# Kernel optimization log

Hardware: AMD Instinct MI355X
Metric: run time of the kernel (lower is better)

Reference implementation:

```python
import jax, jax.numpy as jnp
import numpy as np

V_PATCH_NUMS = (1, 2, 3, 4, 5, 6, 8, 10, 13, 16)


def _pool_matrix(in_size: int, out_size: int) -> jnp.ndarray:
    # Matrix form of torch adaptive_avg_pool1d (== F.interpolate mode='area'):
    # window i averages input bins [floor(i*in/out), ceil((i+1)*in/out)).
    M = np.zeros((out_size, in_size), dtype=np.float32)
    for i in range(out_size):
        s = (i * in_size) // out_size
        e = -((-(i + 1) * in_size) // out_size)  # ceil division
        M[i, s:e] = 1.0 / (e - s)
    return jnp.asarray(M)


def setup_inputs() -> dict:
    key = jax.random.key(0)
    k1, k2 = jax.random.split(key)
    B, C, H, W = 64, 32, 16, 16
    vocab = 4096
    f = jax.random.normal(k1, (B, C, H, W), dtype=jnp.float32)
    # embedding init: uniform(-1/vocab, 1/vocab), as in the torch module
    emb = (jax.random.uniform(k2, (vocab, C), dtype=jnp.float32) * 2.0 - 1.0) / vocab
    return {"f": f, "emb": emb}


def reference(f, emb):
    # Multi-scale residual VQ: per scale -> area-downsample residual,
    # nearest-codebook argmin, embedding gather, bicubic-upsample,
    # accumulate into f_hat and subtract from f_rest.
    B, C, H, W = f.shape
    f = jax.lax.stop_gradient(f)            # f_no_grad in torch
    x = jnp.transpose(f, (0, 2, 3, 1))      # BHWC for resize/gather
    f_rest = x
    f_hat = jnp.zeros_like(x)
    emb_ng = jax.lax.stop_gradient(emb)     # distances use embedding.weight.data
    e_sq = jnp.sum(emb_ng * emb_ng, axis=1)  # [vocab]
    SN = len(V_PATCH_NUMS)
    for si, pn in enumerate(V_PATCH_NUMS):
        last = si == SN - 1
        if last:
            z = f_rest                       # [B,H,W,C]
        else:
            Mh = _pool_matrix(H, pn)
            Mw = _pool_matrix(W, pn)
            z = jnp.einsum('ph,qw,bhwc->bpqc', Mh, Mw, f_rest)  # area interp
        z_NC = z.reshape(-1, C)
        # squared L2 distance to every code: ||z||^2 + ||e||^2 - 2 z e^T
        d = jnp.sum(z_NC * z_NC, axis=1, keepdims=True) + e_sq - 2.0 * (z_NC @ emb_ng.T)
        idx = jnp.argmin(d, axis=1).reshape(B, pn, pn)
        h = emb[idx]                         # [B,pn,pn,C] gather (grad-carrying emb)
        if not last:
            h = jax.image.resize(h, (B, H, W, C), method='cubic')  # bicubic up
        f_hat = f_hat + h
        f_rest = f_rest - h
    return jnp.transpose(f_hat, (0, 3, 1, 2))  # back to BCHW
```

## Files before the change

kernel.cpp:

```cpp
#include <hip/hip_runtime.h>
#include <math.h>

#define WS_ESQ   0
#define WS_STATE 4096
#define WS_FHAT  (4096 + 524288)
#define WS_Z     (4096 + 2*524288)
#define WS_PSC   (4096 + 3*524288)
#define WS_PIX   (4096 + 3*524288 + 131072)

__device__ __forceinline__ float4 v4add(float4 a, float4 b) {
    return make_float4(__fadd_rn(a.x,b.x), __fadd_rn(a.y,b.y),
                       __fadd_rn(a.z,b.z), __fadd_rn(a.w,b.w));
}
__device__ __forceinline__ float4 v4sq(float4 a) {
    return make_float4(__fmul_rn(a.x,a.x), __fmul_rn(a.y,a.y),
                       __fmul_rn(a.z,a.z), __fmul_rn(a.w,a.w));
}
__device__ __forceinline__ float np_pw32(float4 q0, float4 q1, float4 q2, float4 q3,
                                         float4 q4, float4 q5, float4 q6, float4 q7) {
    float4 rA = v4add(v4add(v4add(q0, q2), q4), q6);
    float4 rB = v4add(v4add(v4add(q1, q3), q5), q7);
    float l = __fadd_rn(__fadd_rn(rA.x, rA.y), __fadd_rn(rA.z, rA.w));
    float h = __fadd_rn(__fadd_rn(rB.x, rB.y), __fadd_rn(rB.z, rB.w));
    return __fadd_rn(l, h);
}

__device__ __forceinline__ double keys64(double x) {
    if (x < 1.0)      return ((1.5*x - 2.5)*x)*x + 1.0;
    else if (x < 2.0) return ((-0.5*x + 2.5)*x - 4.0)*x + 2.0;
    return 0.0;
}

__global__ __launch_bounds__(256) void vq_apply(
    const float* __restrict__ f, const float* __restrict__ emb,
    float* __restrict__ esq, float* __restrict__ state, float* __restrict__ fhat,
    float* __restrict__ zws, const float* __restrict__ psc, const int* __restrict__ pix,
    int sIdx, int pn, int pnPrev, int ncbPrev)
{
    __shared__ float fr[1280];
    __shared__ float hs[676];
    __shared__ int   idx_arr[176];
    __shared__ float U[256];
    __shared__ float red_f[1360];
    __shared__ int   red_i[1360];

    const int tid = threadIdx.x;
    const int wg  = blockIdx.x;
    if (wg >= 512) {
        int j = ((wg - 512) << 8) + tid;
        const float4* e4 = (const float4*)(emb + (size_t)j*32);
        esq[j] = np_pw32(v4sq(e4[0]),v4sq(e4[1]),v4sq(e4[2]),v4sq(e4[3]),
                         v4sq(e4[4]),v4sq(e4[5]),v4sq(e4[6]),v4sq(e4[7]));
        return;
    }
    const int b  = wg >> 3;
    const int c0 = (wg & 7) * 4;

    const float* src = (sIdx <= 1) ? f : state;
    for (int o = tid; o < 1024; o += 256) {
        int cc = o >> 8, yx = o & 255;
        fr[yx*5 + cc] = src[b*8192 + (c0 + cc)*256 + yx];
    }
    __syncthreads();

    if (sIdx > 0) {
        const int Vp = pnPrev * pnPrev;
        const int step = ncbPrev >> 3;
        for (int t = tid; t < Vp*8; t += 256) {
            int v = t >> 3, k = t & 7;
            const size_t base = (size_t)((v << 6) + b) * ncbPrev;
            float best = INFINITY; int bi = 0;
            for (int ch = k*step; ch < (k+1)*step; ++ch) {
                float sc = psc[base + ch];
                if (sc < best) { best = sc; bi = pix[base + ch]; }
            }
            red_f[t] = best; red_i[t] = bi;
        }
        __syncthreads();
        if (tid < Vp) {
            float best = INFINITY; int bi = 0;
            for (int k = 0; k < 8; ++k) {
                float sc = red_f[tid*8 + k];
                if (sc < best) { best = sc; bi = red_i[tid*8 + k]; }
            }
            idx_arr[tid] = bi;
        }
        __syncthreads();
        for (int t = tid; t < Vp*4; t += 256)
            hs[t] = emb[(size_t)idx_arr[t >> 2]*32 + c0 + (t & 3)];
        if (tid < 16) {
            double scl = 16.0 / (double)pnPrev;
            double inv = 1.0 / scl;
            double sp = ((double)tid + 0.5) * inv - 0.5;
            double w64[16]; double tot = 0.0;
            for (int q = 0; q < pnPrev; ++q) {
                double wv = keys64(fabs(sp - (double)q));
                w64[q] = wv; tot += wv;
            }
            for (int q = 0; q < pnPrev; ++q) U[tid*16 + q] = (float)(w64[q] / tot);
        }
        __syncthreads();
        {
            const double inv = 1.0 / (16.0 / (double)pnPrev);
            const int yx = tid, y = yx >> 4, x = yx & 15;
            double sy = ((double)y + 0.5) * inv - 0.5;
            double sx = ((double)x + 0.5) * inv - 0.5;
            int p0 = (int)floor(sy) - 1, q0 = (int)floor(sx) - 1;
            int pa = max(0, p0), pb = min(pnPrev - 1, p0 + 3);
            int qa = max(0, q0), qb = min(pnPrev - 1, q0 + 3);
            float acc0 = 0.f, acc1 = 0.f, acc2 = 0.f, acc3 = 0.f;
            for (int p = pa; p <= pb; ++p) {
                float wy = U[y*16 + p];
                for (int q = qa; q <= qb; ++q) {
                    float wx = U[x*16 + q];
                    const float* hp = &hs[(p*pnPrev + q)*4];
                    acc0 = __fadd_rn(acc0, __fmul_rn(__fmul_rn(hp[0], wy), wx));
                    acc1 = __fadd_rn(acc1, __fmul_rn(__fmul_rn(hp[1], wy), wx));
                    acc2 = __fadd_rn(acc2, __fmul_rn(__fmul_rn(hp[2], wy), wx));
                    acc3 = __fadd_rn(acc3, __fmul_rn(__fmul_rn(hp[3], wy), wx));
                }
            }
            float a4[4] = {acc0, acc1, acc2, acc3};
            #pragma unroll
            for (int cc = 0; cc < 4; ++cc) {
                float frv = __fsub_rn(fr[yx*5 + cc], a4[cc]);
                fr[yx*5 + cc] = frv;
                int go = b*8192 + (c0 + cc)*256 + yx;
                state[go] = frv;
                fhat[go] = (sIdx == 1) ? a4[cc] : __fadd_rn(fhat[go], a4[cc]);
            }
        }
        __syncthreads();
    }

    const int V = pn * pn;
    if (pn < 16) {
        if (tid < V) {
            int p = tid / pn, q = tid - p*pn;
            int sh = (p*16)/pn, eh = ((p+1)*16 + pn - 1)/pn;
            int sw = (q*16)/pn, ew = ((q+1)*16 + pn - 1)/pn;
            float Mh = (float)(1.0/(double)(eh - sh));
            float Mw = (float)(1.0/(double)(ew - sw));
            float coef = __fmul_rn(Mh, Mw);
            float a4[4] = {0.f, 0.f, 0.f, 0.f};
            for (int hh = sh; hh < eh; ++hh)
                for (int wy = sw; wy < ew; ++wy) {
                    const float* fp = &fr[(hh*16 + wy)*5];
                    #pragma unroll
                    for (int cc = 0; cc < 4; ++cc)
                        a4[cc] = __fadd_rn(a4[cc], __fmul_rn(coef, fp[cc]));
                }
            *(float4*)(zws + (size_t)((tid << 6) + b)*32 + c0) =
                make_float4(a4[0], a4[1], a4[2], a4[3]);
        }
    } else {
        const int yx = tid;
        *(float4*)(zws + (size_t)((yx << 6) + b)*32 + c0) =
            make_float4(fr[yx*5], fr[yx*5 + 1], fr[yx*5 + 2], fr[yx*5 + 3]);
    }
}

#define LOADZ(P) { \
    const int pr = min((pblk << 8) + (P << 6) + lane, N - 1); \
    const float4* zp = (const float4*)(zws + (size_t)pr*32); \
    z##P##0 = zp[0]; z##P##1 = zp[1]; z##P##2 = zp[2]; z##P##3 = zp[3]; \
    z##P##4 = zp[4]; z##P##5 = zp[5]; z##P##6 = zp[6]; z##P##7 = zp[7]; \
    zsq##P = np_pw32(v4sq(z##P##0),v4sq(z##P##1),v4sq(z##P##2),v4sq(z##P##3), \
                     v4sq(z##P##4),v4sq(z##P##5),v4sq(z##P##6),v4sq(z##P##7)); }

#define FMA4(EV, ZA, ZB, ZC, ZD) \
    acc0 = __fmaf_rn(EV.x, ZA.x, acc0); acc1 = __fmaf_rn(EV.x, ZB.x, acc1); \
    acc2 = __fmaf_rn(EV.x, ZC.x, acc2); acc3 = __fmaf_rn(EV.x, ZD.x, acc3); \
    acc0 = __fmaf_rn(EV.y, ZA.y, acc0); acc1 = __fmaf_rn(EV.y, ZB.y, acc1); \
    acc2 = __fmaf_rn(EV.y, ZC.y, acc2); acc3 = __fmaf_rn(EV.y, ZD.y, acc3); \
    acc0 = __fmaf_rn(EV.z, ZA.z, acc0); acc1 = __fmaf_rn(EV.z, ZB.z, acc1); \
    acc2 = __fmaf_rn(EV.z, ZC.z, acc2); acc3 = __fmaf_rn(EV.z, ZD.z, acc3); \
    acc0 = __fmaf_rn(EV.w, ZA.w, acc0); acc1 = __fmaf_rn(EV.w, ZB.w, acc1); \
    acc2 = __fmaf_rn(EV.w, ZC.w, acc2); acc3 = __fmaf_rn(EV.w, ZD.w, acc3);

__global__ __launch_bounds__(256, 2) void vq_scan(
    const float* __restrict__ emb, const float* __restrict__ esq,
    const float* __restrict__ zws, float* __restrict__ psc, int* __restrict__ pix,
    int V, int ncbMask, int ncbShift, int CB)
{
    __shared__ float ebuf[2][2048];
    __shared__ float esq_l[512];
    __shared__ float red_f[1024];
    __shared__ int   red_i[1024];

    const int tid  = threadIdx.x;
    const int cb   = blockIdx.x & ncbMask;
    const int pblk = blockIdx.x >> ncbShift;
    const int w    = tid >> 6, lane = tid & 63;
    const int N    = V << 6;

    float4 z00,z01,z02,z03,z04,z05,z06,z07; float zsq0;
    float4 z10,z11,z12,z13,z14,z15,z16,z17; float zsq1;
    float4 z20,z21,z22,z23,z24,z25,z26,z27; float zsq2;
    float4 z30,z31,z32,z33,z34,z35,z36,z37; float zsq3;
    LOADZ(0) LOADZ(1) LOADZ(2) LOADZ(3)

    const int jchunk = cb * CB;
    for (int t = tid; t < CB; t += 256) esq_l[t] = esq[jchunk + t];
    const int ntile = CB >> 6;

    {
        const float4* g = (const float4*)(emb + (size_t)jchunk*32);
        for (int t = tid; t < 512; t += 256) ((float4*)ebuf[0])[t] = g[t];
    }
    __syncthreads();

    float best0 = INFINITY, best1 = INFINITY, best2 = INFINITY, best3 = INFINITY;
    int bi0 = 0, bi1 = 0, bi2 = 0, bi3 = 0;

    for (int tile = 0; tile < ntile; ++tile) {
        const int cur = tile & 1;
        if (tile + 1 < ntile) {
            const float4* g = (const float4*)(emb + (size_t)(jchunk + ((tile+1) << 6))*32);
            for (int t = tid; t < 512; t += 256) ((float4*)ebuf[cur ^ 1])[t] = g[t];
        }
        const float* eb = ebuf[cur];
        #pragma unroll 2
        for (int i = 0; i < 16; ++i) {
            const int lc = (w << 4) + i;
            const float4* e4 = (const float4*)(eb + lc*32);
            float acc0 = 0.f, acc1 = 0.f, acc2 = 0.f, acc3 = 0.f;
            float4 ev;
            ev = e4[0]; FMA4(ev, z00, z10, z20, z30)
            ev = e4[1]; FMA4(ev, z01, z11, z21, z31)
            ev = e4[2]; FMA4(ev, z02, z12, z22, z32)
            ev = e4[3]; FMA4(ev, z03, z13, z23, z33)
            ev = e4[4]; FMA4(ev, z04, z14, z24, z34)
            ev = e4[5]; FMA4(ev, z05, z15, z25, z35)
            ev = e4[6]; FMA4(ev, z06, z16, z26, z36)
            ev = e4[7]; FMA4(ev, z07, z17, z27, z37)
            const float sqj = esq_l[(tile << 6) + lc];
            const int j = jchunk + (tile << 6) + lc;
            float d0 = __fsub_rn(__fadd_rn(zsq0, sqj), __fmul_rn(2.0f, acc0));
            float d1 = __fsub_rn(__fadd_rn(zsq1, sqj), __fmul_rn(2.0f, acc1));
            float d2 = __fsub_rn(__fadd_rn(zsq2, sqj), __fmul_rn(2.0f, acc2));
            float d3 = __fsub_rn(__fadd_rn(zsq3, sqj), __fmul_rn(2.0f, acc3));
            if (d0 < best0) { best0 = d0; bi0 = j; }
            if (d1 < best1) { best1 = d1; bi1 = j; }
            if (d2 < best2) { best2 = d2; bi2 = j; }
            if (d3 < best3) { best3 = d3; bi3 = j; }
        }
        __syncthreads();
    }
    red_f[w*256 + lane]       = best0;  red_i[w*256 + lane]       = bi0;
    red_f[w*256 + 64 + lane]  = best1;  red_i[w*256 + 64 + lane]  = bi1;
    red_f[w*256 + 128 + lane] = best2;  red_i[w*256 + 128 + lane] = bi2;
    red_f[w*256 + 192 + lane] = best3;  red_i[w*256 + 192 + lane] = bi3;
    __syncthreads();

    {
        const int p = (pblk << 8) + tid;
        if (p < N) {
            float bb = INFINITY; int bi = 0x7fffffff;
            #pragma unroll
            for (int ww = 0; ww < 4; ++ww) {
                float sc = red_f[ww*256 + tid];
                int   ji = red_i[ww*256 + tid];
                if (sc < bb || (sc == bb && ji < bi)) { bb = sc; bi = ji; }
            }
            psc[(size_t)p*(ncbMask + 1) + cb] = bb;
            pix[(size_t)p*(ncbMask + 1) + cb] = bi;
        }
    }
}

__global__ __launch_bounds__(256) void vq_final(
    const float* __restrict__ emb, const float* __restrict__ fhat,
    const float* __restrict__ psc, const int* __restrict__ pix,
    float* __restrict__ out)
{
    __shared__ int idx_arr[256];
    const int tid = threadIdx.x;
    const int b = blockIdx.x;
    {
        float best = INFINITY; int bi = 0;
        const size_t pb0 = (size_t)((tid << 6) + b) * 8;
        for (int ch = 0; ch < 8; ++ch) {
            float sc = psc[pb0 + ch];
            if (sc < best) { best = sc; bi = pix[pb0 + ch]; }
        }
        idx_arr[tid] = bi;
    }
    __syncthreads();
    for (int o = tid; o < 8192; o += 256) {
        int c = o >> 8, yx = o & 255;
        out[b*8192 + o] = __fadd_rn(fhat[(size_t)b*8192 + o],
                                    emb[(size_t)idx_arr[yx]*32 + c]);
    }
}

extern "C" void kernel_launch(void* const* d_in, const int* in_sizes, int n_in,
                              void* d_out, int out_size, void* d_ws, size_t ws_size,
                              hipStream_t stream) {
    const float* f   = (const float*)d_in[0];
    const float* emb = (const float*)d_in[1];
    float* ws  = (float*)d_ws;
    float* out = (float*)d_out;
    float* esq   = ws + WS_ESQ;
    float* state = ws + WS_STATE;
    float* fhatp = ws + WS_FHAT;
    float* zws   = ws + WS_Z;
    float* psc   = ws + WS_PSC;
    int*   pixp  = (int*)(ws + WS_PIX);
    static const int pns[10]  = {1, 2, 3, 4, 5, 6, 8, 10, 13, 16};
    static const int ncbl[10] = {6, 6, 6, 6, 5, 5, 5, 4, 3, 3};

    for (int s = 0; s < 10; ++s) {
        int pn = pns[s], V = pn*pn, sh = ncbl[s];
        int PB = ((V << 6) + 255) >> 8;
        vq_apply<<<(s == 0) ? 528 : 512, 256, 0, stream>>>(
            f, emb, esq, state, fhatp, zws, psc, pixp,
            s, pn, s > 0 ? pns[s-1] : 0, s > 0 ? (1 << ncbl[s-1]) : 0);
        vq_scan<<<PB << sh, 256, 0, stream>>>(emb, esq, zws, psc, pixp,
                                              V, (1 << sh) - 1, sh, 4096 >> sh);
    }
    vq_final<<<64, 256, 0, stream>>>(emb, fhatp, psc, pixp, out);
}
```

Before: 442.0 us.

## Replace partial-score buffers with packed 64-bit atomicMin argmin reduction

```diff
diff --git a/kernel.cpp b/kernel.cpp
--- a/kernel.cpp
+++ b/kernel.cpp
@@ -5,8 +5,7 @@
 #define WS_STATE 4096
 #define WS_FHAT  (4096 + 524288)
 #define WS_Z     (4096 + 2*524288)
-#define WS_PSC   (4096 + 3*524288)
-#define WS_PIX   (4096 + 3*524288 + 131072)
+#define WS_BEST  (4096 + 3*524288)
 
 __device__ __forceinline__ float4 v4add(float4 a, float4 b) {
     return make_float4(__fadd_rn(a.x,b.x), __fadd_rn(a.y,b.y),
@@ -31,18 +30,22 @@
     return 0.0;
 }
 
+__device__ __forceinline__ unsigned dkey(float d) {
+    unsigned b = __float_as_uint(d);
+    return (b & 0x80000000u) ? ~b : (b | 0x80000000u);
+}
+
 __global__ __launch_bounds__(256) void vq_apply(
     const float* __restrict__ f, const float* __restrict__ emb,
     float* __restrict__ esq, float* __restrict__ state, float* __restrict__ fhat,
-    float* __restrict__ zws, const float* __restrict__ psc, const int* __restrict__ pix,
-    int sIdx, int pn, int pnPrev, int ncbPrev)
+    float* __restrict__ zws, const unsigned long long* __restrict__ bestPrev,
+    unsigned long long* __restrict__ bestCur,
+    int sIdx, int pn, int pnPrev)
 {
     __shared__ float fr[1280];
     __shared__ float hs[676];
     __shared__ int   idx_arr[176];
     __shared__ float U[256];
-    __shared__ float red_f[1360];
-    __shared__ int   red_i[1360];
 
     const int tid = threadIdx.x;
     const int wg  = blockIdx.x;
@@ -56,6 +59,8 @@
     const int b  = wg >> 3;
     const int c0 = (wg & 7) * 4;
 
+    for (int t = tid; t < 32; t += 256) bestCur[wg*32 + t] = ~0ull;
+
     const float* src = (sIdx <= 1) ? f : state;
     for (int o = tid; o < 1024; o += 256) {
         int cc = o >> 8, yx = o & 255;
@@ -65,26 +70,8 @@
 
     if (sIdx > 0) {
         const int Vp = pnPrev * pnPrev;
-        const int step = ncbPrev >> 3;
-        for (int t = tid; t < Vp*8; t += 256) {
-            int v = t >> 3, k = t & 7;
-            const size_t base = (size_t)((v << 6) + b) * ncbPrev;
-            float best = INFINITY; int bi = 0;
-            for (int ch = k*step; ch < (k+1)*step; ++ch) {
-                float sc = psc[base + ch];
-                if (sc < best) { best = sc; bi = pix[base + ch]; }
-            }
-            red_f[t] = best; red_i[t] = bi;
-        }
-        __syncthreads();
-        if (tid < Vp) {
-            float best = INFINITY; int bi = 0;
-            for (int k = 0; k < 8; ++k) {
-                float sc = red_f[tid*8 + k];
-                if (sc < best) { best = sc; bi = red_i[tid*8 + k]; }
-            }
-            idx_arr[tid] = bi;
-        }
+        if (tid < Vp)
+            idx_arr[tid] = (int)(bestPrev[(tid << 6) + b] & 0xFFFFFFFFull);
         __syncthreads();
         for (int t = tid; t < Vp*4; t += 256)
             hs[t] = emb[(size_t)idx_arr[t >> 2]*32 + c0 + (t & 3)];
@@ -180,19 +167,26 @@
 
 __global__ __launch_bounds__(256, 2) void vq_scan(
     const float* __restrict__ emb, const float* __restrict__ esq,
-    const float* __restrict__ zws, float* __restrict__ psc, int* __restrict__ pix,
-    int V, int ncbMask, int ncbShift, int CB)
+    const float* __restrict__ zws, unsigned long long* __restrict__ best, int N)
 {
-    __shared__ float ebuf[2][2048];
-    __shared__ float esq_l[512];
-    __shared__ float red_f[1024];
-    __shared__ int   red_i[1024];
+    __shared__ float ebuf[8192];
+    __shared__ float esq_l[256];
+    float* red_f = ebuf;
+    int*   red_i = (int*)(ebuf + 1024);
 
     const int tid  = threadIdx.x;
-    const int cb   = blockIdx.x & ncbMask;
-    const int pblk = blockIdx.x >> ncbShift;
+    const int cb   = blockIdx.x & 15;
+    const int pblk = blockIdx.x >> 4;
     const int w    = tid >> 6, lane = tid & 63;
-    const int N    = V << 6;
+    const int jchunk = cb << 8;
+
+    {
+        const float4* g = (const float4*)(emb + (size_t)jchunk*32);
+        float4* eb4 = (float4*)ebuf;
+        for (int t = tid; t < 2048; t += 256) eb4[t] = g[t];
+        esq_l[tid] = esq[jchunk + tid];
+    }
+    __syncthreads();
 
     float4 z00,z01,z02,z03,z04,z05,z06,z07; float zsq0;
     float4 z10,z11,z12,z13,z14,z15,z16,z17; float zsq1;
@@ -200,53 +194,35 @@
     float4 z30,z31,z32,z33,z34,z35,z36,z37; float zsq3;
     LOADZ(0) LOADZ(1) LOADZ(2) LOADZ(3)
 
-    const int jchunk = cb * CB;
-    for (int t = tid; t < CB; t += 256) esq_l[t] = esq[jchunk + t];
-    const int ntile = CB >> 6;
-
-    {
-        const float4* g = (const float4*)(emb + (size_t)jchunk*32);
-        for (int t = tid; t < 512; t += 256) ((float4*)ebuf[0])[t] = g[t];
-    }
-    __syncthreads();
-
     float best0 = INFINITY, best1 = INFINITY, best2 = INFINITY, best3 = INFINITY;
     int bi0 = 0, bi1 = 0, bi2 = 0, bi3 = 0;
-
-    for (int tile = 0; tile < ntile; ++tile) {
-        const int cur = tile & 1;
-        if (tile + 1 < ntile) {
-            const float4* g = (const float4*)(emb + (size_t)(jchunk + ((tile+1) << 6))*32);
-            for (int t = tid; t < 512; t += 256) ((float4*)ebuf[cur ^ 1])[t] = g[t];
-        }
-        const float* eb = ebuf[cur];
-        #pragma unroll 2
-        for (int i = 0; i < 16; ++i) {
-            const int lc = (w << 4) + i;
-            const float4* e4 = (const float4*)(eb + lc*32);
-            float acc0 = 0.f, acc1 = 0.f, acc2 = 0.f, acc3 = 0.f;
-            float4 ev;
-            ev = e4[0]; FMA4(ev, z00, z10, z20, z30)
-            ev = e4[1]; FMA4(ev, z01, z11, z21, z31)
-            ev = e4[2]; FMA4(ev, z02, z12, z22, z32)
-            ev = e4[3]; FMA4(ev, z03, z13, z23, z33)
-            ev = e4[4]; FMA4(ev, z04, z14, z24, z34)
-            ev = e4[5]; FMA4(ev, z05, z15, z25, z35)
-            ev = e4[6]; FMA4(ev, z06, z16, z26, z36)
-            ev = e4[7]; FMA4(ev, z07, z17, z27, z37)
-            const float sqj = esq_l[(tile << 6) + lc];
-            const int j = jchunk + (tile << 6) + lc;
-            float d0 = __fsub_rn(__fadd_rn(zsq0, sqj), __fmul_rn(2.0f, acc0));
-            float d1 = __fsub_rn(__fadd_rn(zsq1, sqj), __fmul_rn(2.0f, acc1));
-            float d2 = __fsub_rn(__fadd_rn(zsq2, sqj), __fmul_rn(2.0f, acc2));
-            float d3 = __fsub_rn(__fadd_rn(zsq3, sqj), __fmul_rn(2.0f, acc3));
-            if (d0 < best0) { best0 = d0; bi0 = j; }
-            if (d1 < best1) { best1 = d1; bi1 = j; }
-            if (d2 < best2) { best2 = d2; bi2 = j; }
-            if (d3 < best3) { best3 = d3; bi3 = j; }
-        }
-        __syncthreads();
-    }
+    const int base = w << 6;
+    for (int i = 0; i < 64; ++i) {
+        const int lc = base + i;
+        const float4* e4 = (const float4*)(ebuf + lc*32);
+        float acc0 = 0.f, acc1 = 0.f, acc2 = 0.f, acc3 = 0.f;
+        float4 ev;
+        ev = e4[0]; FMA4(ev, z00, z10, z20, z30)
+        ev = e4[1]; FMA4(ev, z01, z11, z21, z31)
+        ev = e4[2]; FMA4(ev, z02, z12, z22, z32)
+        ev = e4[3]; FMA4(ev, z03, z13, z23, z33)
+        ev = e4[4]; FMA4(ev, z04, z14, z24, z34)
+        ev = e4[5]; FMA4(ev, z05, z15, z25, z35)
+        ev = e4[6]; FMA4(ev, z06, z16, z26, z36)
+        ev = e4[7]; FMA4(ev, z07, z17, z27, z37)
+        const float sqj = esq_l[lc];
+        const int j = jchunk + lc;
+        float d0 = __fsub_rn(__fadd_rn(zsq0, sqj), __fmul_rn(2.0f, acc0));
+        float d1 = __fsub_rn(__fadd_rn(zsq1, sqj), __fmul_rn(2.0f, acc1));
+        float d2 = __fsub_rn(__fadd_rn(zsq2, sqj), __fmul_rn(2.0f, acc2));
+        float d3 = __fsub_rn(__fadd_rn(zsq3, sqj), __fmul_rn(2.0f, acc3));
+        if (d0 < best0) { best0 = d0; bi0 = j; }
+        if (d1 < best1) { best1 = d1; bi1 = j; }
+        if (d2 < best2) { best2 = d2; bi2 = j; }
+        if (d3 < best3) { best3 = d3; bi3 = j; }
+    }
+    __syncthreads();
+
     red_f[w*256 + lane]       = best0;  red_i[w*256 + lane]       = bi0;
     red_f[w*256 + 64 + lane]  = best1;  red_i[w*256 + 64 + lane]  = bi1;
     red_f[w*256 + 128 + lane] = best2;  red_i[w*256 + 128 + lane] = bi2;
@@ -256,36 +232,26 @@
     {
         const int p = (pblk << 8) + tid;
         if (p < N) {
-            float bb = INFINITY; int bi = 0x7fffffff;
+            float bb = INFINITY; int bi = 0;
             #pragma unroll
             for (int ww = 0; ww < 4; ++ww) {
                 float sc = red_f[ww*256 + tid];
-                int   ji = red_i[ww*256 + tid];
-                if (sc < bb || (sc == bb && ji < bi)) { bb = sc; bi = ji; }
-            }
-            psc[(size_t)p*(ncbMask + 1) + cb] = bb;
-            pix[(size_t)p*(ncbMask + 1) + cb] = bi;
+                if (sc < bb) { bb = sc; bi = red_i[ww*256 + tid]; }
+            }
+            unsigned long long pk = ((unsigned long long)dkey(bb) << 32) | (unsigned)bi;
+            atomicMin(&best[p], pk);
         }
     }
 }
 
 __global__ __launch_bounds__(256) void vq_final(
     const float* __restrict__ emb, const float* __restrict__ fhat,
-    const float* __restrict__ psc, const int* __restrict__ pix,
-    float* __restrict__ out)
+    const unsigned long long* __restrict__ best9, float* __restrict__ out)
 {
     __shared__ int idx_arr[256];
     const int tid = threadIdx.x;
     const int b = blockIdx.x;
-    {
-        float best = INFINITY; int bi = 0;
-        const size_t pb0 = (size_t)((tid << 6) + b) * 8;
-        for (int ch = 0; ch < 8; ++ch) {
-            float sc = psc[pb0 + ch];
-            if (sc < best) { best = sc; bi = pix[pb0 + ch]; }
-        }
-        idx_arr[tid] = bi;
-    }
+    idx_arr[tid] = (int)(best9[(tid << 6) + b] & 0xFFFFFFFFull);
     __syncthreads();
     for (int o = tid; o < 8192; o += 256) {
         int c = o >> 8, yx = o & 255;
@@ -305,19 +271,18 @@
     float* state = ws + WS_STATE;
     float* fhatp = ws + WS_FHAT;
     float* zws   = ws + WS_Z;
-    float* psc   = ws + WS_PSC;
-    int*   pixp  = (int*)(ws + WS_PIX);
-    static const int pns[10]  = {1, 2, 3, 4, 5, 6, 8, 10, 13, 16};
-    static const int ncbl[10] = {6, 6, 6, 6, 5, 5, 5, 4, 3, 3};
+    unsigned long long* best = (unsigned long long*)(ws + WS_BEST);
+    static const int pns[10] = {1, 2, 3, 4, 5, 6, 8, 10, 13, 16};
 
     for (int s = 0; s < 10; ++s) {
-        int pn = pns[s], V = pn*pn, sh = ncbl[s];
-        int PB = ((V << 6) + 255) >> 8;
+        int pn = pns[s], V = pn*pn, N = V << 6;
+        int PB = (N + 255) >> 8;
+        unsigned long long* bPrev = best + (size_t)((s + 1) & 1) * 16384;
+        unsigned long long* bCur  = best + (size_t)(s & 1) * 16384;
         vq_apply<<<(s == 0) ? 528 : 512, 256, 0, stream>>>(
-            f, emb, esq, state, fhatp, zws, psc, pixp,
-            s, pn, s > 0 ? pns[s-1] : 0, s > 0 ? (1 << ncbl[s-1]) : 0);
-        vq_scan<<<PB << sh, 256, 0, stream>>>(emb, esq, zws, psc, pixp,
-                                              V, (1 << sh) - 1, sh, 4096 >> sh);
-    }
-    vq_final<<<64, 256, 0, stream>>>(emb, fhatp, psc, pixp, out);
-}
+            f, emb, esq, state, fhatp, zws, bPrev, bCur,
+            s, pn, s > 0 ? pns[s-1] : 0);
+        vq_scan<<<PB * 16, 256, 0, stream>>>(emb, esq, zws, bCur, N);
+    }
+    vq_final<<<64, 256, 0, stream>>>(emb, fhatp, best + 16384, out);
+}
```

After: 433.5 us. Within noise of the previous version (-1.9%).
